# Optimization experiments

Hardware: AMD Instinct MI355X
Metric: run time of the kernel (lower is better)

The kernel has to match this reference:

```python
import jax, jax.numpy as jnp
import numpy as np

N = 100000
E = 1600000
D = 128


def setup_inputs() -> dict:
    key = jax.random.key(0)
    k1, k2, k3 = jax.random.split(key, 3)
    indices = jax.random.randint(k1, (2, E), 0, N, dtype=jnp.int64)
    values = jax.random.normal(k2, (E,), dtype=jnp.float32)
    b = jax.random.normal(k3, (N, D), dtype=jnp.float32)
    return {"indices": indices, "values": values, "n": N, "b": b}


def reference(indices, values, n, b):
    # Sparse COO SpMM: out[r] = sum_{e: row[e]==r} values[e] * b[col[e]]
    row, col = indices[0], indices[1]
    contrib = values[:, None] * b[col]          # [E, D] gather-multiply
    out = jax.ops.segment_sum(contrib, row, num_segments=n)  # [N, D] scatter-add
    return out
```

## Files before the change

### kernel.cpp

```cpp
#include <hip/hip_runtime.h>
#include <hip/hip_fp16.h>


#define D_DIM 128
#define RPB 64
#define RPB_SHIFT 6
#define CRB 256
#define CRB_SHIFT 8
#define MAXCB 512
#define CCAP 4608
#define MAXB 2048
#define CAP_LDS 1408
#define EPT 6
#define EPT1 8
#define OVF_T 8192

typedef float fx4 __attribute__((ext_vector_type(4)));

__global__ __launch_bounds__(256) void convert_b_kernel(
        const float* __restrict__ b, __half* __restrict__ bh, int n8) {
    int i = blockIdx.x * blockDim.x + threadIdx.x;
    if (i >= n8) return;
    const float4* b4 = (const float4*)b;
    float4 a0 = b4[2 * i];
    float4 a1 = b4[2 * i + 1];
    union { __half2 h[4]; uint4 u; } pk;
    pk.h[0] = __floats2half2_rn(a0.x, a0.y);
    pk.h[1] = __floats2half2_rn(a0.z, a0.w);
    pk.h[2] = __floats2half2_rn(a1.x, a1.y);
    pk.h[3] = __floats2half2_rn(a1.z, a1.w);
    ((uint4*)bh)[i] = pk.u;
}

__global__ __launch_bounds__(1024) void p1_coarse(
        const int* __restrict__ rows,
        const int* __restrict__ cols,
        const float* __restrict__ vals,
        int* __restrict__ coarse_cnt,
        int2* __restrict__ coarse,
        int* __restrict__ ovf_cnt,
        int* __restrict__ ovf3,
        int E, int ncb, int ccap, int chunk) {
    __shared__ int hist[MAXCB];
    int tid = threadIdx.x;
    int start = blockIdx.x * chunk;
    int end = start + chunk; if (end > E) end = E;

    for (int i = tid; i < ncb; i += 1024) hist[i] = 0;
    __syncthreads();

    int rr[EPT1]; int cc[EPT1]; float vv[EPT1];
    int ne = 0;
    for (int e = start + tid; e < end; e += 1024) {
        int r = rows[e];
        if (ne < EPT1) { rr[ne] = r; cc[ne] = cols[e]; vv[ne] = vals[e]; }
        ++ne;
        atomicAdd(&hist[r >> CRB_SHIFT], 1);
    }
    __syncthreads();

    for (int bin = tid; bin < ncb; bin += 1024) {
        int c = hist[bin];
        hist[bin] = (c > 0) ? atomicAdd(&coarse_cnt[bin], c) : 0;
    }
    __syncthreads();

    int j = 0;
    for (int e = start + tid; e < end; e += 1024, ++j) {
        int r, c; float v;
        if (j < EPT1) { r = rr[j]; c = cc[j]; v = vv[j]; }
        else          { r = rows[e]; c = cols[e]; v = vals[e]; }
        int bin = r >> CRB_SHIFT;
        int local = atomicAdd(&hist[bin], 1);
        if (local < ccap) {
            coarse[(size_t)bin * ccap + local] =
                make_int2(((r & (CRB - 1)) << 17) | c, __float_as_int(v));
        } else {
            int k = atomicAdd(ovf_cnt, 1);
            if (k < OVF_T) {
                ovf3[3 * k] = r; ovf3[3 * k + 1] = c;
                ovf3[3 * k + 2] = __float_as_int(v);
            }
        }
    }
}

__global__ __launch_bounds__(1024) void p2_fine(
        const int* __restrict__ coarse_cnt,
        const int2* __restrict__ coarse,
        int* __restrict__ bucket_cnt,
        int2* __restrict__ packed,
        int* __restrict__ ovf_cnt,
        int* __restrict__ ovf3,
        int ccap, int cap, int nb) {
    __shared__ int2 stage[CCAP];
    __shared__ int hist4[4];
    __shared__ int loff[5];
    __shared__ int cur[4];

    int bin = blockIdx.x;
    int tid = threadIdx.x;
    int lane = tid & 63;
    int cnt = coarse_cnt[bin];
    if (cnt > ccap) cnt = ccap;
    const int2* cb = coarse + (size_t)bin * ccap;

    if (tid < 4) hist4[tid] = 0;

    int h0 = 0, h1 = 0, h2 = 0, h3 = 0;
    for (int i = tid; i < cnt; i += 1024) {
        int f = (cb[i].x >> 23) & 3;
        h0 += (f == 0); h1 += (f == 1); h2 += (f == 2); h3 += (f == 3);
    }
    for (int off = 32; off; off >>= 1) {
        h0 += __shfl_down(h0, off); h1 += __shfl_down(h1, off);
        h2 += __shfl_down(h2, off); h3 += __shfl_down(h3, off);
    }
    __syncthreads();
    if (lane == 0) {
        atomicAdd(&hist4[0], h0); atomicAdd(&hist4[1], h1);
        atomicAdd(&hist4[2], h2); atomicAdd(&hist4[3], h3);
    }
    __syncthreads();
    if (tid == 0) {
        int o = 0;
        for (int k = 0; k < 4; ++k) { loff[k] = o; cur[k] = o; o += hist4[k]; }
        loff[4] = o;
    }
    __syncthreads();

    for (int i = tid; i < cnt; i += 1024) {
        int2 e = cb[i];
        int f = (e.x >> 23) & 3;
        int p = 0;
        for (int k = 0; k < 4; ++k) {
            unsigned long long m = __ballot(f == k);
            if (f == k) {
                int leader = __ffsll((unsigned long long)m) - 1;
                int base = 0;
                if (lane == leader) base = atomicAdd(&cur[k], (int)__popcll(m));
                base = __shfl(base, leader);
                p = base + (int)__popcll(m & ((1ULL << lane) - 1ULL));
            }
        }
        stage[p] = e;
    }
    __syncthreads();

    int fb0 = bin << (CRB_SHIFT - RPB_SHIFT);
    for (int k = 0; k < 4; ++k) {
        int bkt = fb0 + k;
        if (bkt >= nb) break;
        int s = loff[k];
        int run = loff[k + 1] - s;
        int w = (run > cap) ? cap : run;
        for (int i = tid; i < w; i += 1024) {
            int2 e = stage[s + i];
            packed[(size_t)bkt * cap + i] = make_int2(e.x & 0x7FFFFF, e.y);
        }
        if (tid == 0) bucket_cnt[bkt] = w;
        for (int i = cap + tid; i < run; i += 1024) {
            int2 e = stage[s + i];
            int k2 = atomicAdd(ovf_cnt, 1);
            if (k2 < OVF_T) {
                int r = (bin << CRB_SHIFT) | ((unsigned)e.x >> 17);
                ovf3[3 * k2] = r; ovf3[3 * k2 + 1] = e.x & 0x1FFFF;
                ovf3[3 * k2 + 2] = e.y;
            }
        }
    }
}

template <bool HALF>
__global__ __launch_bounds__(256) void phase2_sort_gather(
        const int* __restrict__ bucket_cnt,
        const int2* __restrict__ packed,
        const __half* __restrict__ bh,
        const float* __restrict__ b,
        float* __restrict__ out,
        int cap, int N) {
    __shared__ int2 sorted[CAP_LDS];
    __shared__ int hist[RPB];
    __shared__ int offs[RPB + 1];
    __shared__ int cursor[RPB];

    int bucket = blockIdx.x;
    int tid = threadIdx.x;

    int cnt = bucket_cnt[bucket];
    if (cnt > cap) cnt = cap;
    const int2* pk = packed + (size_t)bucket * cap;

    if (tid < RPB) hist[tid] = 0;
    __syncthreads();

    int2 ev[EPT];
    int  rl[EPT];
    int ne = 0;
    for (int i = tid; i < cnt; i += 256) {
        int2 e = pk[i];
        ev[ne] = e;
        rl[ne] = ((unsigned)e.x) >> 17;
        atomicAdd(&hist[rl[ne]], 1);
        ++ne;
    }
    __syncthreads();

    for (int d = 1; d < RPB; d <<= 1) {
        int t = (tid < RPB && tid >= d) ? hist[tid - d] : 0;
        __syncthreads();
        if (tid < RPB) hist[tid] += t;
        __syncthreads();
    }
    if (tid == 0) offs[0] = 0;
    if (tid < RPB) {
        offs[tid + 1] = hist[tid];
        cursor[tid] = (tid == 0) ? 0 : hist[tid - 1];
    }
    __syncthreads();

    for (int j = 0; j < ne; ++j) {
        int pos = atomicAdd(&cursor[rl[j]], 1);
        sorted[pos] = make_int2(ev[j].x & 0x1FFFF, ev[j].y);
    }
    __syncthreads();

    int g = tid >> 5;
    int glane = tid & 31;
    int r0 = bucket << RPB_SHIFT;
    for (int k = 0; k < 8; ++k) {
        int rr = g * 8 + k;
        int start = offs[rr];
        int num = offs[rr + 1] - start;
        float4 acc = make_float4(0.f, 0.f, 0.f, 0.f);
        for (int base = 0; base < num; base += 8) {
#pragma unroll
            for (int j = 0; j < 8; ++j) {
                int idx = base + j;
                int sidx = start + ((idx < num) ? idx : (num - 1));
                int2 e = sorted[sidx];
                float v = (idx < num) ? __int_as_float(e.y) : 0.f;
                if (HALF) {
                    uint2 hv = ((const uint2*)(bh + (size_t)e.x * D_DIM))[glane];
                    __half2* hp = (__half2*)&hv;
                    float2 f0 = __half22float2(hp[0]);
                    float2 f1 = __half22float2(hp[1]);
                    acc.x += v * f0.x;
                    acc.y += v * f0.y;
                    acc.z += v * f1.x;
                    acc.w += v * f1.y;
                } else {
                    float4 bv = ((const float4*)(b + (size_t)e.x * D_DIM))[glane];
                    acc.x += v * bv.x;
                    acc.y += v * bv.y;
                    acc.z += v * bv.z;
                    acc.w += v * bv.w;
                }
            }
        }
        int r = r0 + rr;
        if (r < N) {
            fx4 av = {acc.x, acc.y, acc.z, acc.w};
            __builtin_nontemporal_store(av, (fx4*)(out + (size_t)r * D_DIM) + glane);
        }
    }
}

__global__ __launch_bounds__(1024) void phase1_partition(
        const int* __restrict__ rows,
        const int* __restrict__ cols,
        const float* __restrict__ vals,
        int* __restrict__ bucket_cnt,
        int2* __restrict__ packed,
        int* __restrict__ ovf_cnt,
        int* __restrict__ ovf3,
        int E, int nb, int cap, int chunk) {
    __shared__ int hist[MAXB];
    int tid = threadIdx.x;
    int start = blockIdx.x * chunk;
    int end = start + chunk; if (end > E) end = E;

    for (int i = tid; i < nb; i += 1024) hist[i] = 0;
    __syncthreads();

    int rr[EPT1]; int cc[EPT1]; float vv[EPT1];
    int ne = 0;
    for (int e = start + tid; e < end; e += 1024) {
        int r = rows[e];
        if (ne < EPT1) { rr[ne] = r; cc[ne] = cols[e]; vv[ne] = vals[e]; }
        ++ne;
        atomicAdd(&hist[r >> RPB_SHIFT], 1);
    }
    __syncthreads();

    for (int bkt = tid; bkt < nb; bkt += 1024) {
        int c = hist[bkt];
        hist[bkt] = (c > 0) ? atomicAdd(&bucket_cnt[bkt], c) : 0;
    }
    __syncthreads();

    int j = 0;
    for (int e = start + tid; e < end; e += 1024, ++j) {
        int r, c; float v;
        if (j < EPT1) { r = rr[j]; c = cc[j]; v = vv[j]; }
        else          { r = rows[e]; c = cols[e]; v = vals[e]; }
        int bkt = r >> RPB_SHIFT;
        int local = atomicAdd(&hist[bkt], 1);
        if (local < cap) {
            int key = ((r & (RPB - 1)) << 17) | c;
            packed[(size_t)bkt * cap + local] = make_int2(key, __float_as_int(v));
        } else {
            int k = atomicAdd(ovf_cnt, 1);
            if (k < OVF_T) {
                ovf3[3 * k] = r; ovf3[3 * k + 1] = c;
                ovf3[3 * k + 2] = __float_as_int(v);
            }
        }
    }
}

__global__ void fixup_kernel(const int* __restrict__ ovf_cnt,
                             const int* __restrict__ ovf3,
                             const float* __restrict__ b,
                             float* __restrict__ out) {
    int items = *ovf_cnt;
    if (items > OVF_T) items = OVF_T;
    int gsz  = (gridDim.x * blockDim.x) >> 5;
    int gid  = (blockIdx.x * blockDim.x + threadIdx.x) >> 5;
    int lane = threadIdx.x & 31;
    for (int i = gid; i < items; i += gsz) {
        int r = ovf3[3 * i];
        int c = ovf3[3 * i + 1];
        float v = __int_as_float(ovf3[3 * i + 2]);
        float4 bv = ((const float4*)(b + (size_t)c * D_DIM))[lane];
        float* op = out + (size_t)r * D_DIM + (size_t)lane * 4;
        atomicAdd(op + 0, v * bv.x);
        atomicAdd(op + 1, v * bv.y);
        atomicAdd(op + 2, v * bv.z);
        atomicAdd(op + 3, v * bv.w);
    }
}

__global__ void spmm_atomic_kernel(const int* __restrict__ rows,
                                   const int* __restrict__ cols,
                                   const float* __restrict__ vals,
                                   const float* __restrict__ b,
                                   float* __restrict__ out, int E) {
    int t = blockIdx.x * blockDim.x + threadIdx.x;
    int e = t >> 5;
    if (e >= E) return;
    int lane = t & 31;
    int r = rows[e];
    int c = cols[e];
    float v = vals[e];
    float4 bv = ((const float4*)(b + (size_t)c * D_DIM))[lane];
    float* op = out + (size_t)r * D_DIM + (size_t)lane * 4;
    atomicAdd(op + 0, v * bv.x);
    atomicAdd(op + 1, v * bv.y);
    atomicAdd(op + 2, v * bv.z);
    atomicAdd(op + 3, v * bv.w);
}

extern "C" void kernel_launch(void* const* d_in, const int* in_sizes, int n_in,
                              void* d_out, int out_size, void* d_ws, size_t ws_size,
                              hipStream_t stream) {
    const int*   indices = (const int*)d_in[0];
    const float* vals    = (const float*)d_in[1];
    const float* b       = (const float*)d_in[3];
    float*       out     = (float*)d_out;

    int E = in_sizes[1];
    int N = out_size / D_DIM;
    const int* rows = indices;
    const int* cols = indices + E;

    int nb  = (N + RPB - 1) >> RPB_SHIFT;
    int ncb = (N + CRB - 1) >> CRB_SHIFT;
    int avg  = (nb  > 0) ? E / nb  : 0;
    int cavg = (ncb > 0) ? E / ncb : 0;
    int cap = CAP_LDS;
    size_t bh_bytes = (size_t)N * D_DIM * 2;
    int n8 = N * D_DIM / 8;

    {
        bool ok = (ncb <= MAXCB) && (N <= 131072) &&
                  (cavg + cavg / 8 <= CCAP) && (cap > avg + avg / 8);
        size_t fixedN = (size_t)ncb * 4 + (size_t)nb * 4 + 4 + (size_t)OVF_T * 12;
        size_t pk_off = (fixedN + 255) & ~(size_t)255;
        size_t un_off = (pk_off + (size_t)nb * cap * 8 + 255) & ~(size_t)255;
        size_t coarse_bytes = (size_t)ncb * CCAP * 8;
        size_t un_bytes = coarse_bytes > bh_bytes ? coarse_bytes : bh_bytes;
        if (ok && ws_size >= un_off + un_bytes) {
            char* w = (char*)d_ws;
            int*    coarse_cnt = (int*)w;
            int*    bucket_cnt = (int*)(w + (size_t)ncb * 4);
            int*    ovf_cnt    = (int*)(w + (size_t)ncb * 4 + (size_t)nb * 4);
            int*    ovf3       = (int*)(w + (size_t)ncb * 4 + (size_t)nb * 4 + 4);
            int2*   packed     = (int2*)(w + pk_off);
            int2*   coarse     = (int2*)(w + un_off);
            __half* bh         = (__half*)(w + un_off);

            (void)hipMemsetAsync(coarse_cnt, 0,
                                 (size_t)ncb * 4 + (size_t)nb * 4 + 4, stream);

            const int P1_WGS = 256;
            int chunk = (E + P1_WGS - 1) / P1_WGS;
            p1_coarse<<<P1_WGS, 1024, 0, stream>>>(
                rows, cols, vals, coarse_cnt, coarse, ovf_cnt, ovf3,
                E, ncb, CCAP, chunk);

            p2_fine<<<ncb, 1024, 0, stream>>>(
                coarse_cnt, coarse, bucket_cnt, packed, ovf_cnt, ovf3,
                CCAP, cap, nb);

            convert_b_kernel<<<(n8 + 255) / 256, 256, 0, stream>>>(b, bh, n8);

            phase2_sort_gather<true><<<nb, 256, 0, stream>>>(
                bucket_cnt, packed, bh, b, out, cap, N);

            fixup_kernel<<<8, 256, 0, stream>>>(ovf_cnt, ovf3, b, out);
            return;
        }
    }

    size_t fixed      = (size_t)nb * 4 + 4 + (size_t)OVF_T * 12;
    size_t bh_off     = (fixed + 255) & ~(size_t)255;
    size_t packed_h   = (bh_off + bh_bytes + 255) & ~(size_t)255;
    size_t packed_f   = bh_off;
    size_t need_h     = packed_h + (size_t)nb * cap * 8;
    size_t need_f     = packed_f + (size_t)nb * cap * 8;

    bool okBase = (nb <= MAXB) && (N <= 131072) && (cap > avg + avg / 8);
    bool useHalf = okBase && (ws_size >= need_h);
    bool useF32  = okBase && !useHalf && (ws_size >= need_f);

    if (!useHalf && !useF32) {
        (void)hipMemsetAsync(d_out, 0, (size_t)out_size * sizeof(float), stream);
        long long total = (long long)E * 32;
        int blocks = (int)((total + 255) / 256);
        spmm_atomic_kernel<<<blocks, 256, 0, stream>>>(rows, cols, vals, b, out, E);
        return;
    }

    char* w = (char*)d_ws;
    int*    bucket_cnt = (int*)w;
    int*    ovf_cnt    = (int*)(w + (size_t)nb * 4);
    int*    ovf3       = (int*)(w + (size_t)nb * 4 + 4);
    __half* bh         = (__half*)(w + bh_off);
    int2*   packed     = (int2*)(w + (useHalf ? packed_h : packed_f));

    (void)hipMemsetAsync(bucket_cnt, 0, (size_t)nb * 4 + 4, stream);

    if (useHalf)
        convert_b_kernel<<<(n8 + 255) / 256, 256, 0, stream>>>(b, bh, n8);

    const int P1_WGS = 256;
    int chunk = (E + P1_WGS - 1) / P1_WGS;
    phase1_partition<<<P1_WGS, 1024, 0, stream>>>(
        rows, cols, vals, bucket_cnt, packed, ovf_cnt, ovf3, E, nb, cap, chunk);

    if (useHalf)
        phase2_sort_gather<true><<<nb, 256, 0, stream>>>(
            bucket_cnt, packed, bh, b, out, cap, N);
    else
        phase2_sort_gather<false><<<nb, 256, 0, stream>>>(
            bucket_cnt, packed, bh, b, out, cap, N);

    fixup_kernel<<<8, 256, 0, stream>>>(ovf_cnt, ovf3, b, out);
}
```

Before: 228.2 us.

## Locally sort edges by coarse bucket in LDS before coalesced scatter

The first binning pass now uses fixed 4096-edge chunks per workgroup (more workgroups). Each workgroup prefix-scans its bucket histogram, counting-sorts its edges into an LDS stage, and then writes them to the global coarse buckets in contiguous runs. The aim is to replace scattered per-edge global writes with coalesced ones and to cut the number of global atomics per edge. The cost is extra LDS traffic, a serial log-step scan with barriers, and a smaller register cache of edges.

Result: faster. 216.9 us (-5.0%).

```diff
diff --git a/kernel.cpp b/kernel.cpp
--- a/kernel.cpp
+++ b/kernel.cpp
@@ -13,6 +13,8 @@
 #define CAP_LDS 1408
 #define EPT 6
 #define EPT1 8
+#define CHUNK1 4096
+#define EPC 4
 #define OVF_T 8192
 
 typedef float fx4 __attribute__((ext_vector_type(4)));
@@ -32,7 +34,7 @@
     ((uint4*)bh)[i] = pk.u;
 }
 
-__global__ __launch_bounds__(1024) void p1_coarse(
+__global__ __launch_bounds__(1024) void p1_sortcoarse(
         const int* __restrict__ rows,
         const int* __restrict__ cols,
         const float* __restrict__ vals,
@@ -40,46 +42,71 @@
         int2* __restrict__ coarse,
         int* __restrict__ ovf_cnt,
         int* __restrict__ ovf3,
-        int E, int ncb, int ccap, int chunk) {
+        int E, int ncb, int ccap) {
     __shared__ int hist[MAXCB];
+    __shared__ int cursor[MAXCB];
+    __shared__ int2 stage[CHUNK1];
+    __shared__ unsigned short sbkt[CHUNK1];
+
     int tid = threadIdx.x;
-    int start = blockIdx.x * chunk;
-    int end = start + chunk; if (end > E) end = E;
+    int start = blockIdx.x * CHUNK1;
+    int end = start + CHUNK1; if (end > E) end = E;
+    int n = end - start;
 
     for (int i = tid; i < ncb; i += 1024) hist[i] = 0;
     __syncthreads();
 
-    int rr[EPT1]; int cc[EPT1]; float vv[EPT1];
+    int rr[EPC]; int cc[EPC]; float vv[EPC];
     int ne = 0;
     for (int e = start + tid; e < end; e += 1024) {
         int r = rows[e];
-        if (ne < EPT1) { rr[ne] = r; cc[ne] = cols[e]; vv[ne] = vals[e]; }
+        if (ne < EPC) { rr[ne] = r; cc[ne] = cols[e]; vv[ne] = vals[e]; }
         ++ne;
         atomicAdd(&hist[r >> CRB_SHIFT], 1);
     }
     __syncthreads();
 
-    for (int bin = tid; bin < ncb; bin += 1024) {
-        int c = hist[bin];
-        hist[bin] = (c > 0) ? atomicAdd(&coarse_cnt[bin], c) : 0;
-    }
-    __syncthreads();
-
-    int j = 0;
-    for (int e = start + tid; e < end; e += 1024, ++j) {
+    for (int d = 1; d < ncb; d <<= 1) {
+        int t = (tid < ncb && tid >= d) ? hist[tid - d] : 0;
+        __syncthreads();
+        if (tid < ncb && tid >= d) hist[tid] += t;
+        __syncthreads();
+    }
+
+    int incl = 0, excl = 0;
+    if (tid < ncb) { incl = hist[tid]; excl = tid ? hist[tid - 1] : 0; }
+    __syncthreads();
+    if (tid < ncb) {
+        int cnt = incl - excl;
+        cursor[tid] = excl;
+        int gres = (cnt > 0) ? atomicAdd(&coarse_cnt[tid], cnt) : 0;
+        hist[tid] = gres - excl;
+    }
+    __syncthreads();
+
+    for (int j = 0; j < ne; ++j) {
         int r, c; float v;
-        if (j < EPT1) { r = rr[j]; c = cc[j]; v = vv[j]; }
-        else          { r = rows[e]; c = cols[e]; v = vals[e]; }
-        int bin = r >> CRB_SHIFT;
-        int local = atomicAdd(&hist[bin], 1);
-        if (local < ccap) {
-            coarse[(size_t)bin * ccap + local] =
-                make_int2(((r & (CRB - 1)) << 17) | c, __float_as_int(v));
+        if (j < EPC) { r = rr[j]; c = cc[j]; v = vv[j]; }
+        else { int e = start + tid + j * 1024; r = rows[e]; c = cols[e]; v = vals[e]; }
+        int bkt = r >> CRB_SHIFT;
+        int pos = atomicAdd(&cursor[bkt], 1);
+        stage[pos] = make_int2(((r & (CRB - 1)) << 17) | c, __float_as_int(v));
+        sbkt[pos] = (unsigned short)bkt;
+    }
+    __syncthreads();
+
+    for (int i = tid; i < n; i += 1024) {
+        int bkt = sbkt[i];
+        int2 e = stage[i];
+        int gidx = i + hist[bkt];
+        if (gidx < ccap) {
+            coarse[(size_t)bkt * ccap + gidx] = e;
         } else {
             int k = atomicAdd(ovf_cnt, 1);
             if (k < OVF_T) {
-                ovf3[3 * k] = r; ovf3[3 * k + 1] = c;
-                ovf3[3 * k + 2] = __float_as_int(v);
+                int r = (bkt << CRB_SHIFT) | ((unsigned)e.x >> 17);
+                ovf3[3 * k] = r; ovf3[3 * k + 1] = e.x & 0x1FFFF;
+                ovf3[3 * k + 2] = e.y;
             }
         }
     }
@@ -403,11 +430,10 @@
             (void)hipMemsetAsync(coarse_cnt, 0,
                                  (size_t)ncb * 4 + (size_t)nb * 4 + 4, stream);
 
-            const int P1_WGS = 256;
-            int chunk = (E + P1_WGS - 1) / P1_WGS;
-            p1_coarse<<<P1_WGS, 1024, 0, stream>>>(
+            int nwg1 = (E + CHUNK1 - 1) / CHUNK1;
+            p1_sortcoarse<<<nwg1, 1024, 0, stream>>>(
                 rows, cols, vals, coarse_cnt, coarse, ovf_cnt, ovf3,
-                E, ncb, CCAP, chunk);
+                E, ncb, CCAP);
 
             p2_fine<<<ncb, 1024, 0, stream>>>(
                 coarse_cnt, coarse, bucket_cnt, packed, ovf_cnt, ovf3,
```
